# Optimization experiments

Measured on AMD Instinct MI355X. Metric: run time of the kernel, lower is better.

The kernel has to match this reference:

```python
import math
import jax, jax.numpy as jnp
import numpy as np

N_HEADS = 2


def _scatter_softmax(scores, seg, num_segments):
    # softmax over edges grouped by destination (head) node, per attention head
    m = jax.ops.segment_max(scores, seg, num_segments=num_segments)  # [N, H]
    e = jnp.exp(scores - m[seg])
    s = jax.ops.segment_sum(e, seg, num_segments=num_segments)  # [N, H]
    return e / s[seg]


def _l2norm(x, eps=1e-12):
    # torch F.normalize(dim=1)
    n = jnp.sqrt(jnp.sum(x * x, axis=1, keepdims=True))
    return x / jnp.maximum(n, eps)


def setup_inputs() -> dict:
    key = jax.random.key(0)
    ks = jax.random.split(key, 8)
    dims, n_relations = 128, 10
    n_users, n_entities = 30000, 60000
    n_edges, n_inter = 600000, 800000
    user_emb = jax.random.normal(ks[0], (n_users, dims), dtype=jnp.float32)
    entity_emb = jax.random.normal(ks[1], (n_entities, dims), dtype=jnp.float32)
    inter_edge = jnp.stack([
        jax.random.randint(ks[2], (n_inter,), 0, n_users),
        jax.random.randint(ks[3], (n_inter,), 0, n_entities),
    ], axis=0)
    inter_edge_w = jax.random.uniform(ks[4], (n_inter,), dtype=jnp.float32)
    edge_index = jax.random.randint(ks[5], (2, n_edges), 0, n_entities)
    edge_type = jax.random.randint(ks[6], (n_edges,), 1, n_relations + 1)  # 1-based
    relation_emb = 0.1 * jax.random.normal(ks[7], (n_relations, dims), dtype=jnp.float32)
    W_Q = 0.1 * jax.random.normal(jax.random.fold_in(key, 99), (dims, dims), dtype=jnp.float32)
    return {"layers_num": 2, "user_emb": user_emb, "entity_emb": entity_emb,
            "inter_edge": inter_edge, "inter_edge_w": inter_edge_w,
            "edge_index": edge_index, "edge_type": edge_type,
            "relation_emb": relation_emb, "W_Q": W_Q}


def reference(layers_num, user_emb, entity_emb, inter_edge, inter_edge_w,
              edge_index, edge_type, relation_emb, W_Q):
    dims = entity_emb.shape[1]
    d_k = dims // N_HEADS
    n_entities = entity_emb.shape[0]
    n_users = user_emb.shape[0]
    head, tail = edge_index[0], edge_index[1]
    rel = relation_emb[edge_type - 1]  # [E, D]
    rel_h = rel.reshape(-1, N_HEADS, d_k)
    u_idx, i_idx = inter_edge[0], inter_edge[1]

    def agg_layer(u_emb, e_emb):
        head_emb = e_emb[head]                                   # [E, D]
        tail_emb = e_emb[tail]                                   # [E, D]
        q = (head_emb @ W_Q).reshape(-1, N_HEADS, d_k)
        k = (tail_emb @ W_Q).reshape(-1, N_HEADS, d_k) * rel_h
        score = jnp.sum(q * k, axis=-1) / math.sqrt(d_k)          # [E, H]
        attn = _scatter_softmax(score, head, n_entities)          # [E, H]
        value = (tail_emb * rel).reshape(-1, N_HEADS, d_k)
        weighted = (value * attn[..., None]).reshape(-1, dims)
        entity_agg = jax.ops.segment_sum(weighted, head, num_segments=n_entities)
        entity_agg = _l2norm(entity_agg)
        item_agg = inter_edge_w[:, None] * e_emb[i_idx]           # [Ei, D]
        user_agg = jax.ops.segment_sum(item_agg, u_idx, num_segments=n_users)
        return entity_agg, user_agg

    user_embs = [user_emb]
    entity_embs = [entity_emb]
    for _ in range(layers_num):
        entity_emb, user_emb = agg_layer(user_emb, entity_emb)
        user_embs.append(user_emb)
        entity_embs.append(entity_emb)
    user_out = jnp.mean(jnp.stack(user_embs, axis=1), axis=1)
    entity_out = jnp.mean(jnp.stack(entity_embs, axis=1), axis=1)
    return (user_out, entity_out)
```

## Files before the change

### kernel.cpp

```cpp
#include <hip/hip_runtime.h>
#include <hip/hip_bf16.h>

#define D 128
typedef unsigned short u16;
typedef unsigned int u32;

__device__ __forceinline__ float bf2f(u16 u) {
    return __uint_as_float(((u32)u) << 16);
}
__device__ __forceinline__ u16 f2bf(float f) {
    union { float f; u32 u; } a; a.f = f;
    u32 r = (a.u + 0x7FFF + ((a.u >> 16) & 1)) >> 16;
    return (u16)r;
}
__device__ __forceinline__ float2 bf2x2(u32 v) {
    float2 r;
    r.x = __uint_as_float(v << 16);
    r.y = __uint_as_float(v & 0xFFFF0000u);
    return r;
}
__device__ __forceinline__ u32 packbf2(float a, float b) {
    return (u32)f2bf(a) | ((u32)f2bf(b) << 16);
}
__device__ __forceinline__ float ldIn(const void* p, size_t i, int isBf) {
    return isBf ? bf2f(((const u16*)p)[i]) : ((const float*)p)[i];
}
__device__ __forceinline__ void stOut(void* p, size_t i, float v, int isBf) {
    if (isBf) ((u16*)p)[i] = f2bf(v);
    else      ((float*)p)[i] = v;
}

__global__ void sniff_k(const u16* __restrict__ probe, int* __restrict__ flag) {
    int t = threadIdx.x;
    u16 v = probe[2 * t];
    int ex = (v >> 7) & 0xFF;
    int sane = (ex == 0) || (ex >= 0x70 && ex <= 0x8A);
    unsigned long long m = __ballot(sane != 0);
    if (t == 0) *flag = (__popcll(m) >= 48) ? 1 : 0;
}

__global__ void convert_k(const void* __restrict__ src, u16* __restrict__ dst,
                          int n, const int* __restrict__ flagp) {
    int i = blockIdx.x * blockDim.x + threadIdx.x;
    int isBf = *flagp;
    if (i < n) dst[i] = isBf ? ((const u16*)src)[i] : f2bf(((const float*)src)[i]);
}

__global__ void zero_k(int* __restrict__ p, int n) {
    int i = blockIdx.x * blockDim.x + threadIdx.x;
    if (i < n) p[i] = 0;
}
__global__ void hist_k(const int* __restrict__ keys, int n, int nDst,
                       int* __restrict__ cntP1) {
    int i = blockIdx.x * blockDim.x + threadIdx.x;
    if (i < n) {
        int k = min(max(keys[i], 0), nDst - 1);
        atomicAdd(&cntP1[k + 1], 1);
    }
}
__global__ void copy_k(const int* __restrict__ src, int* __restrict__ dst, int n) {
    int i = blockIdx.x * blockDim.x + threadIdx.x;
    if (i < n) dst[i] = src[i];
}
__global__ void scatter_e(const int* __restrict__ head, const int* __restrict__ tail,
                          const int* __restrict__ etyp, int n, int nDst, int nEnt,
                          int* __restrict__ pos, int* __restrict__ pack) {
    int i = blockIdx.x * blockDim.x + threadIdx.x;
    if (i < n) {
        int k = min(max(head[i], 0), nDst - 1);
        int p = atomicAdd(&pos[k], 1);
        if (p >= 0 && p < n) {
            int tl = min(max(tail[i], 0), nEnt - 1);
            int rt = min(max(etyp[i] - 1, 0), 9);
            pack[p] = tl | (rt << 24);
        }
    }
}
__global__ void scatter_u(const int* __restrict__ u_idx, const int* __restrict__ i_idx,
                          const void* __restrict__ iw, int n, int nDst, int nEnt,
                          int* __restrict__ pos, int* __restrict__ item,
                          float* __restrict__ wt, const int* __restrict__ flagp) {
    int i = blockIdx.x * blockDim.x + threadIdx.x;
    int isBf = *flagp;
    if (i < n) {
        int k = min(max(u_idx[i], 0), nDst - 1);
        int p = atomicAdd(&pos[k], 1);
        if (p >= 0 && p < n) {
            item[p] = min(max(i_idx[i], 0), nEnt - 1);
            wt[p] = ldIn(iw, i, isBf);
        }
    }
}

__global__ __launch_bounds__(256) void block_sum_k(const int* __restrict__ buf, int n,
                                                   int* __restrict__ bsum) {
    __shared__ int waveTot[4];
    int b = blockIdx.x, t = threadIdx.x, lane = t & 63, wave = t >> 6;
    int idx = 1 + b * 1024 + t * 4;
    int s = 0;
    #pragma unroll
    for (int k = 0; k < 4; ++k)
        if (idx + k <= n) s += buf[idx + k];
    #pragma unroll
    for (int o = 32; o > 0; o >>= 1) s += __shfl_xor(s, o);
    if (lane == 0) waveTot[wave] = s;
    __syncthreads();
    if (t == 0) bsum[b] = waveTot[0] + waveTot[1] + waveTot[2] + waveTot[3];
}
__global__ void scan_bsums_k(int* __restrict__ bsum, int nb) {
    int t = threadIdx.x;
    int v = (t < nb) ? bsum[t] : 0;
    int x = v;
    #pragma unroll
    for (int o = 1; o < 64; o <<= 1) {
        int y = __shfl_up(x, o);
        if (t >= o) x += y;
    }
    if (t < nb) bsum[t] = x - v;
}
__global__ __launch_bounds__(256) void block_scan_k(int* __restrict__ buf, int n,
                                                    const int* __restrict__ bsum) {
    __shared__ int waveTot[4];
    int b = blockIdx.x, t = threadIdx.x, lane = t & 63, wave = t >> 6;
    int idx = 1 + b * 1024 + t * 4;
    int v0 = 0, v1 = 0, v2 = 0, v3 = 0;
    if (idx     <= n) v0 = buf[idx];
    if (idx + 1 <= n) v1 = buf[idx + 1];
    if (idx + 2 <= n) v2 = buf[idx + 2];
    if (idx + 3 <= n) v3 = buf[idx + 3];
    int s = v0 + v1 + v2 + v3;
    int x = s;
    #pragma unroll
    for (int o = 1; o < 64; o <<= 1) {
        int y = __shfl_up(x, o);
        if (lane >= o) x += y;
    }
    if (lane == 63) waveTot[wave] = x;
    __syncthreads();
    int off = bsum[b];
    for (int wv = 0; wv < wave; ++wv) off += waveTot[wv];
    int r0 = off + (x - s) + v0;
    int r1 = r0 + v1;
    int r2 = r1 + v2;
    int r3 = r2 + v3;
    if (idx     <= n) buf[idx]     = r0;
    if (idx + 1 <= n) buf[idx + 1] = r1;
    if (idx + 2 <= n) buf[idx + 2] = r2;
    if (idx + 3 <= n) buf[idx + 3] = r3;
}

#define GEMM_ROWS 64
#define WSTRIDE 132
__global__ __launch_bounds__(128) void gemm_P2(const u16* __restrict__ E,
                                               const u16* __restrict__ WQ,
                                               u16* __restrict__ P, int nRows) {
    __shared__ u16 sWT[D * WSTRIDE];
    __shared__ float sRow[4][D];
    int t = threadIdx.x;
    for (int i = t; i < D * D; i += 128) {
        int k = i >> 7, c = i & 127;
        sWT[c * WSTRIDE + k] = WQ[i];
    }
    int r0 = blockIdx.x * GEMM_ROWS;
    int rEnd = min(r0 + GEMM_ROWS, nRows);
    __syncthreads();
    const u32* E32 = (const u32*)E;
    for (int r = r0; r < rEnd; r += 4) {
        for (int i = t; i < 256; i += 128) {
            int row = i >> 6, c2 = i & 63;
            float2 f = make_float2(0.f, 0.f);
            if (r + row < nRows) f = bf2x2(E32[(size_t)(r + row) * 64 + c2]);
            sRow[row][2 * c2] = f.x;
            sRow[row][2 * c2 + 1] = f.y;
        }
        __syncthreads();
        float a0 = 0.f, a1 = 0.f, a2 = 0.f, a3 = 0.f;
        const u16* wcol = &sWT[t * WSTRIDE];
        #pragma unroll 4
        for (int k = 0; k < D; k += 4) {
            ushort4 wv = *(const ushort4*)(wcol + k);
            float w0 = bf2f(wv.x), w1 = bf2f(wv.y), w2 = bf2f(wv.z), w3 = bf2f(wv.w);
            float4 rA = *(const float4*)&sRow[0][k];
            float4 rB = *(const float4*)&sRow[1][k];
            float4 rC = *(const float4*)&sRow[2][k];
            float4 rD2 = *(const float4*)&sRow[3][k];
            a0 += rA.x * w0 + rA.y * w1 + rA.z * w2 + rA.w * w3;
            a1 += rB.x * w0 + rB.y * w1 + rB.z * w2 + rB.w * w3;
            a2 += rC.x * w0 + rC.y * w1 + rC.z * w2 + rC.w * w3;
            a3 += rD2.x * w0 + rD2.y * w1 + rD2.z * w2 + rD2.w * w3;
        }
        if (r + 0 < nRows) P[(size_t)(r + 0) * D + t] = f2bf(a0);
        if (r + 1 < nRows) P[(size_t)(r + 1) * D + t] = f2bf(a1);
        if (r + 2 < nRows) P[(size_t)(r + 2) * D + t] = f2bf(a2);
        if (r + 3 < nRows) P[(size_t)(r + 3) * D + t] = f2bf(a3);
        __syncthreads();
    }
}

__global__ __launch_bounds__(256) void entity_agg3(
    const u16* __restrict__ P, const u16* __restrict__ eCur,
    const u16* __restrict__ relb, const int* __restrict__ e_off,
    const int* __restrict__ e_pack, void* __restrict__ eOut,
    const u32* __restrict__ e0b, int finalMode, size_t outElemOff,
    int nEnt, const int* __restrict__ flagp) {
    __shared__ u16 sRel[10 * D];
    int tid = threadIdx.x;
    for (int i = tid; i < 10 * D; i += 256) sRel[i] = relb[i];
    __syncthreads();
    int wid = (blockIdx.x * blockDim.x + tid) >> 6;
    int lane = tid & 63;
    if (wid >= nEnt) return;
    const u32* P32 = (const u32*)P;
    const u32* E32 = (const u32*)eCur;
    const u32* R32 = (const u32*)sRel;
    float2 q = bf2x2(P32[(size_t)wid * 64 + lane]);
    const float SC = 0.125f * 1.44269504f;
    float l = 0.f, a0 = 0.f, a1 = 0.f;
    int s = e_off[wid], e = e_off[wid + 1];
    for (int j0 = s; j0 < e; j0 += 64) {
        int B = min(64, e - j0);
        int pk = (lane < B) ? e_pack[j0 + lane] : 0;
        int pv = __shfl(pk, 0);
        size_t off = (size_t)(pv & 0xFFFFFF) * 64 + lane;
        u32 ptv = P32[off];
        u32 evv = E32[off];
        for (int i = 0; i < B; ++i) {
            u32 cpt = ptv, cev = evv;
            int cpv = pv;
            if (i + 1 < B) {
                pv = __shfl(pk, i + 1);
                off = (size_t)(pv & 0xFFFFFF) * 64 + lane;
                ptv = P32[off];
                evv = E32[off];
            }
            int rt = (int)((u32)cpv >> 24);
            float2 rr = bf2x2(R32[rt * 64 + lane]);
            float2 pt = bf2x2(cpt);
            float2 ev = bf2x2(cev);
            float v0 = ev.x * rr.x;
            float v1 = ev.y * rr.y;
            float prod = q.x * pt.x * rr.x + q.y * pt.y * rr.y;
            #pragma unroll
            for (int o = 16; o > 0; o >>= 1) prod += __shfl_xor(prod, o);
            float p = exp2f(prod * SC);
            l += p;
            a0 = fmaf(p, v0, a0);
            a1 = fmaf(p, v1, a1);
        }
    }
    float o0 = (l > 0.f) ? a0 / l : 0.f;
    float o1 = (l > 0.f) ? a1 / l : 0.f;
    float ss = o0 * o0 + o1 * o1;
    #pragma unroll
    for (int o = 32; o > 0; o >>= 1) ss += __shfl_xor(ss, o);
    float inv = 1.f / fmaxf(sqrtf(ss), 1e-12f);
    float w0 = o0 * inv, w1 = o1 * inv;
    size_t b32i = (size_t)wid * 64 + lane;
    if (finalMode) {
        int isBf = *flagp;
        const float k = 1.0f / 3.0f;
        size_t be = 2 * b32i;
        float2 ec = bf2x2(E32[b32i]);
        float2 e0 = bf2x2(e0b[b32i]);
        w0 = (e0.x + ec.x + w0) * k;
        w1 = (e0.y + ec.y + w1) * k;
        stOut(eOut, outElemOff + be, w0, isBf);
        stOut(eOut, outElemOff + be + 1, w1, isBf);
    } else {
        ((u32*)eOut)[b32i] = packbf2(w0, w1);
    }
}

__global__ __launch_bounds__(256) void user_agg3(
    const u16* __restrict__ eCur, const int* __restrict__ u_off,
    const int* __restrict__ u_item, const float* __restrict__ u_wt,
    float* __restrict__ usum, const void* __restrict__ ueRaw,
    void* __restrict__ outU, int finalMode, int nU, int nEnt,
    const int* __restrict__ flagp) {
    int wid = (blockIdx.x * blockDim.x + threadIdx.x) >> 6;
    int lane = threadIdx.x & 63;
    if (wid >= nU) return;
    const u32* E32 = (const u32*)eCur;
    float a0 = 0.f, a1 = 0.f;
    int s = u_off[wid], e = u_off[wid + 1];
    for (int j0 = s; j0 < e; j0 += 64) {
        int B = min(64, e - j0);
        int it = (lane < B) ? u_item[j0 + lane] : 0;
        float wv = (lane < B) ? u_wt[j0 + lane] : 0.f;
        int i0 = __shfl(it, 0);
        u32 ev0 = E32[(size_t)i0 * 64 + lane];
        u32 ev1 = 0;
        if (B > 1) {
            int i1 = __shfl(it, 1);
            ev1 = E32[(size_t)i1 * 64 + lane];
        }
        for (int i = 0; i < B; ++i) {
            u32 cur = ev0;
            ev0 = ev1;
            if (i + 2 < B) {
                int nx = __shfl(it, i + 2);
                ev1 = E32[(size_t)nx * 64 + lane];
            }
            float wc = __shfl(wv, i);
            float2 f = bf2x2(cur);
            a0 = fmaf(wc, f.x, a0);
            a1 = fmaf(wc, f.y, a1);
        }
    }
    size_t b32i = (size_t)wid * 64 + lane;
    if (finalMode) {
        int isBf = *flagp;
        const float k = 1.0f / 3.0f;
        size_t be = 2 * b32i;
        float2 us = ((const float2*)usum)[b32i];
        stOut(outU, be, (ldIn(ueRaw, be, isBf) + us.x + a0) * k, isBf);
        stOut(outU, be + 1, (ldIn(ueRaw, be + 1, isBf) + us.y + a1) * k, isBf);
    } else {
        ((float2*)usum)[b32i] = make_float2(a0, a1);
    }
}

extern "C" void kernel_launch(void* const* d_in, const int* in_sizes, int n_in,
                              void* d_out, int out_size, void* d_ws, size_t ws_size,
                              hipStream_t stream) {
    const void* ue  = d_in[1];
    const void* ee  = d_in[2];
    const int*  itr = (const int*)d_in[3];
    const void* iw  = d_in[4];
    const int*  eix = (const int*)d_in[5];
    const int*  ety = (const int*)d_in[6];
    const void* rel = d_in[7];
    const void* wq  = d_in[8];

    const int nU = in_sizes[1] / D;
    const int nE = in_sizes[2] / D;
    const int Ei = in_sizes[4];
    const int Ee = in_sizes[6];
    const int nRel = in_sizes[7] / D;

    const int* u_idx = itr;
    const int* i_idx = itr + Ei;
    const int* head  = eix;
    const int* tail  = eix + Ee;

    char* w = (char*)d_ws;
    auto alloc = [&](size_t bytes) {
        char* p = w;
        w += (bytes + 255) & ~(size_t)255;
        return p;
    };
    int*   flag  = (int*)alloc(256);
    int*  e_off  = (int*)alloc((size_t)(nE + 1) * 4);
    int*  u_off  = (int*)alloc((size_t)(nU + 1) * 4);
    int*  e_pos  = (int*)alloc((size_t)nE * 4);
    int*  u_pos  = (int*)alloc((size_t)nU * 4);
    int*  e_pack = (int*)alloc((size_t)Ee * 4);
    int*  u_item = (int*)alloc((size_t)Ei * 4);
    float* u_wt  = (float*)alloc((size_t)Ei * 4);
    int*  bsumE  = (int*)alloc(64 * 4);
    int*  bsumU  = (int*)alloc(64 * 4);
    u16*  eeb    = (u16*)alloc((size_t)nE * D * 2);
    u16*  wqb    = (u16*)alloc((size_t)D * D * 2);
    u16*  relb   = (u16*)alloc((size_t)nRel * D * 2);
    u16*  eL1    = (u16*)alloc((size_t)nE * D * 2);
    u16*  P      = (u16*)alloc((size_t)nE * D * 2);
    float* usum  = (float*)alloc((size_t)nU * D * 4);

    if ((size_t)(w - (char*)d_ws) > ws_size) {
        return;
    }

    sniff_k<<<1, 64, 0, stream>>>((const u16*)ue, flag);

    convert_k<<<(nE * D + 255) / 256, 256, 0, stream>>>(ee, eeb, nE * D, flag);
    convert_k<<<(D * D + 255) / 256, 256, 0, stream>>>(wq, wqb, D * D, flag);
    convert_k<<<(nRel * D + 255) / 256, 256, 0, stream>>>(rel, relb, nRel * D, flag);

    const int nbE = (nE + 1023) / 1024;
    const int nbU = (nU + 1023) / 1024;
    zero_k<<<(nE + 1 + 255) / 256, 256, 0, stream>>>(e_off, nE + 1);
    zero_k<<<(nU + 1 + 255) / 256, 256, 0, stream>>>(u_off, nU + 1);
    hist_k<<<(Ee + 255) / 256, 256, 0, stream>>>(head, Ee, nE, e_off);
    hist_k<<<(Ei + 255) / 256, 256, 0, stream>>>(u_idx, Ei, nU, u_off);
    block_sum_k<<<nbE, 256, 0, stream>>>(e_off, nE, bsumE);
    block_sum_k<<<nbU, 256, 0, stream>>>(u_off, nU, bsumU);
    scan_bsums_k<<<1, 64, 0, stream>>>(bsumE, nbE);
    scan_bsums_k<<<1, 64, 0, stream>>>(bsumU, nbU);
    block_scan_k<<<nbE, 256, 0, stream>>>(e_off, nE, bsumE);
    block_scan_k<<<nbU, 256, 0, stream>>>(u_off, nU, bsumU);
    copy_k<<<(nE + 255) / 256, 256, 0, stream>>>(e_off, e_pos, nE);
    copy_k<<<(nU + 255) / 256, 256, 0, stream>>>(u_off, u_pos, nU);
    scatter_e<<<(Ee + 255) / 256, 256, 0, stream>>>(head, tail, ety, Ee, nE, nE,
                                                    e_pos, e_pack);
    scatter_u<<<(Ei + 255) / 256, 256, 0, stream>>>(u_idx, i_idx, iw, Ei, nU, nE,
                                                    u_pos, u_item, u_wt, flag);

    const int entBlocks  = (nE * 64 + 255) / 256;
    const int userBlocks = (nU * 64 + 255) / 256;
    const int gemmBlocks = (nE + GEMM_ROWS - 1) / GEMM_ROWS;

    gemm_P2<<<gemmBlocks, 128, 0, stream>>>(eeb, wqb, P, nE);
    entity_agg3<<<entBlocks, 256, 0, stream>>>(P, eeb, relb, e_off, e_pack,
                                               eL1, nullptr, 0, 0, nE, flag);
    user_agg3<<<userBlocks, 256, 0, stream>>>(eeb, u_off, u_item, u_wt,
                                              usum, nullptr, nullptr, 0, nU, nE, flag);

    gemm_P2<<<gemmBlocks, 128, 0, stream>>>(eL1, wqb, P, nE);
    entity_agg3<<<entBlocks, 256, 0, stream>>>(P, eL1, relb, e_off, e_pack,
                                               d_out, (const u32*)eeb, 1,
                                               (size_t)nU * D, nE, flag);
    user_agg3<<<userBlocks, 256, 0, stream>>>(eL1, u_off, u_item, u_wt,
                                              usum, ue, d_out, 1, nU, nE, flag);
}
```

Before: 701.1 us.

## Replace scalar FP32 projection GEMM with MFMA bf16 matrix-core kernel

The per-layer entity projection E@W_Q, previously computed with scalar FMAs over rows staged in shared memory, now uses the 16x16x32 bf16 MFMA instruction. Each wave computes a 16-row tile across all 128 output columns. A fragments are loaded straight from global memory and B fragments come from a transposed, padded copy of W_Q in shared memory. This targets the compute-bound GEMM portion of the pipeline. Output writes are scattered 2-byte stores per lane, which may be less coalesced.

New measurement: 564.9 us. 19.4% less time.

```diff
diff --git a/kernel.cpp b/kernel.cpp
--- a/kernel.cpp
+++ b/kernel.cpp
@@ -150,50 +150,43 @@
 }
 
 #define GEMM_ROWS 64
-#define WSTRIDE 132
-__global__ __launch_bounds__(128) void gemm_P2(const u16* __restrict__ E,
+#define WT_STRIDE 136
+typedef __attribute__((ext_vector_type(8))) short bf16x8;
+typedef __attribute__((ext_vector_type(4))) float f32x4;
+
+__global__ __launch_bounds__(256) void gemm_P3(const u16* __restrict__ E,
                                                const u16* __restrict__ WQ,
                                                u16* __restrict__ P, int nRows) {
-    __shared__ u16 sWT[D * WSTRIDE];
-    __shared__ float sRow[4][D];
+    __shared__ u16 sWT[D * WT_STRIDE];
     int t = threadIdx.x;
-    for (int i = t; i < D * D; i += 128) {
+    for (int i = t; i < D * D; i += 256) {
         int k = i >> 7, c = i & 127;
-        sWT[c * WSTRIDE + k] = WQ[i];
-    }
-    int r0 = blockIdx.x * GEMM_ROWS;
-    int rEnd = min(r0 + GEMM_ROWS, nRows);
+        sWT[c * WT_STRIDE + k] = WQ[i];
+    }
     __syncthreads();
-    const u32* E32 = (const u32*)E;
-    for (int r = r0; r < rEnd; r += 4) {
-        for (int i = t; i < 256; i += 128) {
-            int row = i >> 6, c2 = i & 63;
-            float2 f = make_float2(0.f, 0.f);
-            if (r + row < nRows) f = bf2x2(E32[(size_t)(r + row) * 64 + c2]);
-            sRow[row][2 * c2] = f.x;
-            sRow[row][2 * c2 + 1] = f.y;
-        }
-        __syncthreads();
-        float a0 = 0.f, a1 = 0.f, a2 = 0.f, a3 = 0.f;
-        const u16* wcol = &sWT[t * WSTRIDE];
-        #pragma unroll 4
-        for (int k = 0; k < D; k += 4) {
-            ushort4 wv = *(const ushort4*)(wcol + k);
-            float w0 = bf2f(wv.x), w1 = bf2f(wv.y), w2 = bf2f(wv.z), w3 = bf2f(wv.w);
-            float4 rA = *(const float4*)&sRow[0][k];
-            float4 rB = *(const float4*)&sRow[1][k];
-            float4 rC = *(const float4*)&sRow[2][k];
-            float4 rD2 = *(const float4*)&sRow[3][k];
-            a0 += rA.x * w0 + rA.y * w1 + rA.z * w2 + rA.w * w3;
-            a1 += rB.x * w0 + rB.y * w1 + rB.z * w2 + rB.w * w3;
-            a2 += rC.x * w0 + rC.y * w1 + rC.z * w2 + rC.w * w3;
-            a3 += rD2.x * w0 + rD2.y * w1 + rD2.z * w2 + rD2.w * w3;
-        }
-        if (r + 0 < nRows) P[(size_t)(r + 0) * D + t] = f2bf(a0);
-        if (r + 1 < nRows) P[(size_t)(r + 1) * D + t] = f2bf(a1);
-        if (r + 2 < nRows) P[(size_t)(r + 2) * D + t] = f2bf(a2);
-        if (r + 3 < nRows) P[(size_t)(r + 3) * D + t] = f2bf(a3);
-        __syncthreads();
+    int wave = t >> 6, lane = t & 63;
+    int m = lane & 15, quad = lane >> 4;
+    int row0 = blockIdx.x * GEMM_ROWS + wave * 16;
+    int rowA = min(row0 + m, nRows - 1);
+    const u16* erow = E + (size_t)rowA * D;
+    bf16x8 afrag[4];
+    #pragma unroll
+    for (int ks = 0; ks < 4; ++ks)
+        afrag[ks] = *(const bf16x8*)(erow + ks * 32 + quad * 8);
+    #pragma unroll
+    for (int ct = 0; ct < 8; ++ct) {
+        f32x4 acc = {0.f, 0.f, 0.f, 0.f};
+        const u16* wcol = sWT + (ct * 16 + m) * WT_STRIDE + quad * 8;
+        #pragma unroll
+        for (int ks = 0; ks < 4; ++ks) {
+            bf16x8 bfrag = *(const bf16x8*)(wcol + ks * 32);
+            acc = __builtin_amdgcn_mfma_f32_16x16x32_bf16(afrag[ks], bfrag, acc, 0, 0, 0);
+        }
+        #pragma unroll
+        for (int reg = 0; reg < 4; ++reg) {
+            int r = row0 + quad * 4 + reg;
+            if (r < nRows) P[(size_t)r * D + ct * 16 + m] = f2bf(acc[reg]);
+        }
     }
 }
 
@@ -399,13 +392,13 @@
     const int userBlocks = (nU * 64 + 255) / 256;
     const int gemmBlocks = (nE + GEMM_ROWS - 1) / GEMM_ROWS;
 
-    gemm_P2<<<gemmBlocks, 128, 0, stream>>>(eeb, wqb, P, nE);
+    gemm_P3<<<gemmBlocks, 256, 0, stream>>>(eeb, wqb, P, nE);
     entity_agg3<<<entBlocks, 256, 0, stream>>>(P, eeb, relb, e_off, e_pack,
                                                eL1, nullptr, 0, 0, nE, flag);
     user_agg3<<<userBlocks, 256, 0, stream>>>(eeb, u_off, u_item, u_wt,
                                               usum, nullptr, nullptr, 0, nU, nE, flag);
 
-    gemm_P2<<<gemmBlocks, 128, 0, stream>>>(eL1, wqb, P, nE);
+    gemm_P3<<<gemmBlocks, 256, 0, stream>>>(eL1, wqb, P, nE);
     entity_agg3<<<entBlocks, 256, 0, stream>>>(P, eL1, relb, e_off, e_pack,
                                                d_out, (const u32*)eeb, 1,
                                                (size_t)nU * D, nE, flag);
```
